# Kernel tuning notes

Measured on AMD Instinct MI355X. Metric: run time of the kernel, lower is better.

## Reference

```python
import math
import jax, jax.numpy as jnp
import numpy as np

E = 1024
H = 16
HD = E // H
MLP = 4 * E
EPS = 1e-6


def setup_inputs() -> dict:
    key = jax.random.key(0)
    ks = jax.random.split(key, 12)
    s = lambda fan_in: 1.0 / math.sqrt(fan_in)
    return {
        "x": jax.random.normal(ks[0], (8, 1024, E), dtype=jnp.float32),
        "ln1_g": jnp.ones((E,), jnp.float32),
        "ln1_b": jnp.zeros((E,), jnp.float32),
        "w_qkv": jax.random.normal(ks[1], (E, 3 * E), jnp.float32) * s(E),
        "b_qkv": jnp.zeros((3 * E,), jnp.float32),
        "w_o": jax.random.normal(ks[2], (E, E), jnp.float32) * s(E),
        "b_o": jnp.zeros((E,), jnp.float32),
        "ln2_g": jnp.ones((E,), jnp.float32),
        "ln2_b": jnp.zeros((E,), jnp.float32),
        "w_fc1": jax.random.normal(ks[3], (E, MLP), jnp.float32) * s(E),
        "b_fc1": jnp.zeros((MLP,), jnp.float32),
        "w_fc2": jax.random.normal(ks[4], (MLP, E), jnp.float32) * s(MLP),
        "b_fc2": jnp.zeros((E,), jnp.float32),
    }


def _layernorm(x, g, b):
    mu = jnp.mean(x, axis=-1, keepdims=True)
    var = jnp.mean(jnp.square(x - mu), axis=-1, keepdims=True)
    return (x - mu) * jax.lax.rsqrt(var + EPS) * g + b


def _attn(x, w_qkv, b_qkv, w_o, b_o):
    B, N, _ = x.shape
    qkv = (x @ w_qkv + b_qkv).reshape(B, N, 3, H, HD)
    q, k, v = qkv[:, :, 0], qkv[:, :, 1], qkv[:, :, 2]  # [B,N,H,HD]
    scores = jnp.einsum("bnhd,bmhd->bhnm", q, k) / math.sqrt(HD)
    probs = jax.nn.softmax(scores, axis=-1)
    out = jnp.einsum("bhnm,bmhd->bnhd", probs, v).reshape(B, N, H * HD)
    return out @ w_o + b_o


def reference(x, ln1_g, ln1_b, w_qkv, b_qkv, w_o, b_o, ln2_g, ln2_b,
              w_fc1, b_fc1, w_fc2, b_fc2):
    # pre-LN attention block with residual
    x = x + _attn(_layernorm(x, ln1_g, ln1_b), w_qkv, b_qkv, w_o, b_o)
    # pre-LN MLP block with residual (exact GELU, matching torch nn.GELU)
    h = _layernorm(x, ln2_g, ln2_b) @ w_fc1 + b_fc1
    h = jax.nn.gelu(h, approximate=False)
    x = x + (h @ w_fc2 + b_fc2)
    return x
```

## Files before the change

kernel.cpp:

```cpp
#include <hip/hip_runtime.h>
#include <stdint.h>

typedef unsigned short u16;
typedef __bf16 bf16x8 __attribute__((ext_vector_type(8)));
typedef float f32x4 __attribute__((ext_vector_type(4)));

#define GLD16(gp, lp) __builtin_amdgcn_global_load_lds( \
    (__attribute__((address_space(1))) void*)(uintptr_t)(gp), \
    (__attribute__((address_space(3))) void*)(uintptr_t)(lp), 16, 0, 0)

#define MM(a, b, c) __builtin_amdgcn_mfma_f32_16x16x32_bf16(a, b, c, 0, 0, 0)

__device__ __forceinline__ u16 f2bf(float f) {
  uint32_t u = __builtin_bit_cast(uint32_t, f);
  u += 0x7FFFu + ((u >> 16) & 1u);
  return (u16)(u >> 16);
}

__global__ __launch_bounds__(256) void wtrans(const float* __restrict__ w,
                                              u16* __restrict__ wt, int K, int Nn) {
  __shared__ float tile[64][68];
  const int c0 = blockIdx.x << 6, r0 = blockIdx.y << 6;
  const int t = threadIdx.x, tr = t >> 2, tc = t & 3;
#pragma unroll
  for (int p = 0; p < 4; ++p) {
    float4 v = *(const float4*)&w[(size_t)(r0 + tr) * Nn + c0 + tc * 4 + p * 16];
    tile[tr][tc * 4 + p * 16 + 0] = v.x;
    tile[tr][tc * 4 + p * 16 + 1] = v.y;
    tile[tr][tc * 4 + p * 16 + 2] = v.z;
    tile[tr][tc * 4 + p * 16 + 3] = v.w;
  }
  __syncthreads();
#pragma unroll
  for (int p = 0; p < 4; ++p) {
    u16 e0 = f2bf(tile[tc * 4 + p * 16 + 0][tr]);
    u16 e1 = f2bf(tile[tc * 4 + p * 16 + 1][tr]);
    u16 e2 = f2bf(tile[tc * 4 + p * 16 + 2][tr]);
    u16 e3 = f2bf(tile[tc * 4 + p * 16 + 3][tr]);
    uint2 o;
    o.x = (uint32_t)e0 | ((uint32_t)e1 << 16);
    o.y = (uint32_t)e2 | ((uint32_t)e3 << 16);
    *(uint2*)&wt[(size_t)(c0 + tr) * K + r0 + tc * 4 + p * 16] = o;
  }
}

__global__ __launch_bounds__(256) void lnorm(const float* x, const float* __restrict__ g,
                                             const float* __restrict__ bta,
                                             u16* __restrict__ out) {
  const int lane = threadIdx.x & 63, wid = threadIdx.x >> 6;
  const size_t token = (size_t)blockIdx.x * 4 + wid;
  const float* row = x + token * 1024;
  float v[16];
#pragma unroll
  for (int i = 0; i < 4; ++i) {
    float4 f = *(const float4*)&row[(lane + i * 64) * 4];
    v[i * 4 + 0] = f.x; v[i * 4 + 1] = f.y; v[i * 4 + 2] = f.z; v[i * 4 + 3] = f.w;
  }
  float s = 0.f, s2 = 0.f;
#pragma unroll
  for (int i = 0; i < 16; ++i) { s += v[i]; s2 += v[i] * v[i]; }
  for (int off = 1; off < 64; off <<= 1) {
    s += __shfl_xor(s, off);
    s2 += __shfl_xor(s2, off);
  }
  const float mu = s * (1.0f / 1024.0f);
  const float var = s2 * (1.0f / 1024.0f) - mu * mu;
  const float rstd = rsqrtf(var + 1e-6f);
  u16* orow = out + token * 1024;
#pragma unroll
  for (int i = 0; i < 4; ++i) {
    const int c = (lane + i * 64) * 4;
    float4 gv = *(const float4*)&g[c];
    float4 bv = *(const float4*)&bta[c];
    u16 e0 = f2bf((v[i * 4 + 0] - mu) * rstd * gv.x + bv.x);
    u16 e1 = f2bf((v[i * 4 + 1] - mu) * rstd * gv.y + bv.y);
    u16 e2 = f2bf((v[i * 4 + 2] - mu) * rstd * gv.z + bv.z);
    u16 e3 = f2bf((v[i * 4 + 3] - mu) * rstd * gv.w + bv.w);
    uint2 o;
    o.x = (uint32_t)e0 | ((uint32_t)e1 << 16);
    o.y = (uint32_t)e2 | ((uint32_t)e3 << 16);
    *(uint2*)&orow[c] = o;
  }
}

template <int EPI>
__global__ __launch_bounds__(256, 2) void g97(const u16* __restrict__ A,
                                              const u16* __restrict__ Bt,
                                              const float* __restrict__ bias,
                                              const float* res, void* Cout,
                                              int Ndim, int K, float qscale,
                                              int qlimit, int gn) {
  __shared__ __align__(16) u16 lds[2][16384];
  const int tid = threadIdx.x, lane = tid & 63, wid = tid >> 6;
  const int wm = wid & 1, wn = wid >> 1;

  const int wg = blockIdx.x;
  const int swz = (wg & 7) * ((int)gridDim.x >> 3) + (wg >> 3);
  const int mblk = swz / gn, nb = swz - mblk * gn;
  const int m0 = mblk << 7, n0 = nb << 7;

  const int srow = tid >> 3;
  const int schunk = (tid & 7) ^ (srow & 7);
  const u16* Ag = A + (size_t)(m0 + srow) * K + schunk * 8;
  const u16* Bg = Bt + (size_t)(n0 + srow) * K + schunk * 8;
  const size_t rstep = (size_t)32 * K;
  char* lb = (char*)&lds[0][0];

  const int rrow = lane & 15, g = lane >> 4;
  const int ph0 = (g ^ (rrow & 7)) * 16;
  const int aoff0 = (wm * 64 + rrow) * 128 + ph0;
  const int aoff1 = (wm * 64 + rrow) * 128 + (ph0 ^ 64);
  const int boff0 = 16384 + (wn * 64 + rrow) * 128 + ph0;
  const int boff1 = 16384 + (wn * 64 + rrow) * 128 + (ph0 ^ 64);

  const f32x4 fzero = {0.f, 0.f, 0.f, 0.f};
  f32x4 acc[4][4];
#pragma unroll
  for (int i = 0; i < 4; ++i)
#pragma unroll
    for (int j = 0; j < 4; ++j) acc[i][j] = fzero;

#define STG(kt, s) do { \
    char* d_ = lb + (s) * 32768; \
    const u16* a_ = Ag + (size_t)(kt) * 64; \
    const u16* b_ = Bg + (size_t)(kt) * 64; \
    GLD16(a_,             d_ + tid * 16); \
    GLD16(a_ + rstep,     d_ + 4096 + tid * 16); \
    GLD16(a_ + 2 * rstep, d_ + 8192 + tid * 16); \
    GLD16(a_ + 3 * rstep, d_ + 12288 + tid * 16); \
    GLD16(b_,             d_ + 16384 + tid * 16); \
    GLD16(b_ + rstep,     d_ + 20480 + tid * 16); \
    GLD16(b_ + 2 * rstep, d_ + 24576 + tid * 16); \
    GLD16(b_ + 3 * rstep, d_ + 28672 + tid * 16); \
  } while (0)

  const int nk = K >> 6;
  STG(0, 0);
  __syncthreads();
  for (int kt = 0; kt < nk; ++kt) {
    if (kt + 1 < nk) STG(kt + 1, (kt + 1) & 1);
    const char* sb = lb + (kt & 1) * 32768;
    bf16x8 af[4], bfr[4];
#pragma unroll
    for (int mf = 0; mf < 4; ++mf)
      af[mf] = *(const bf16x8*)(sb + aoff0 + mf * 2048);
#pragma unroll
    for (int nf = 0; nf < 4; ++nf)
      bfr[nf] = *(const bf16x8*)(sb + boff0 + nf * 2048);
#pragma unroll
    for (int mf = 0; mf < 4; ++mf)
#pragma unroll
      for (int nf = 0; nf < 4; ++nf)
        acc[mf][nf] = MM(af[mf], bfr[nf], acc[mf][nf]);
#pragma unroll
    for (int mf = 0; mf < 4; ++mf)
      af[mf] = *(const bf16x8*)(sb + aoff1 + mf * 2048);
#pragma unroll
    for (int nf = 0; nf < 4; ++nf)
      bfr[nf] = *(const bf16x8*)(sb + boff1 + nf * 2048);
#pragma unroll
    for (int mf = 0; mf < 4; ++mf)
#pragma unroll
      for (int nf = 0; nf < 4; ++nf)
        acc[mf][nf] = MM(af[mf], bfr[nf], acc[mf][nf]);
    __syncthreads();
  }
#undef STG

  const int g4 = (lane >> 4) << 2;
#pragma unroll
  for (int nf = 0; nf < 4; ++nf) {
    const int col = n0 + wn * 64 + nf * 16 + rrow;
    const float bvb = bias[col];
    const float csf = (EPI == 0 && col < qlimit) ? qscale : 1.0f;
#pragma unroll
    for (int mf = 0; mf < 4; ++mf) {
#pragma unroll
      for (int r = 0; r < 4; ++r) {
        const int row = m0 + wm * 64 + mf * 16 + g4 + r;
        float v = acc[mf][nf][r] + bvb;
        if (EPI == 0) v *= csf;
        if (EPI == 1) v = 0.5f * v * (1.0f + erff(v * 0.70710678118654752f));
        if (EPI == 2) {
          v += res[(size_t)row * Ndim + col];
          ((float*)Cout)[(size_t)row * Ndim + col] = v;
        } else {
          ((u16*)Cout)[(size_t)row * Ndim + col] = f2bf(v);
        }
      }
    }
  }
}

__global__ __launch_bounds__(256) void vtrans(const u16* __restrict__ qkv,
                                              u16* __restrict__ vt) {
  const int bh = blockIdx.y, b = bh >> 4, h = bh & 15;
  const int n0 = blockIdx.x << 6;
  __shared__ __align__(16) u16 tile[64][72];
  const int t = threadIdx.x, r = t >> 2, c = t & 3;
  const u16* src = qkv + (size_t)((b << 10) + n0 + r) * 3072 + 2048 + (h << 6);
#pragma unroll
  for (int p = 0; p < 2; ++p)
    *(uint4*)&tile[r][(c * 2 + p) * 8] = *(const uint4*)(src + (c * 2 + p) * 8);
  __syncthreads();
  u16* dst = vt + (size_t)((bh << 6) + r) * 1024 + n0;
#pragma unroll
  for (int p = 0; p < 2; ++p) {
    u16 o[8];
#pragma unroll
    for (int j = 0; j < 8; ++j) o[j] = tile[(c * 2 + p) * 8 + j][r];
    uint4 w;
    w.x = (uint32_t)o[0] | ((uint32_t)o[1] << 16);
    w.y = (uint32_t)o[2] | ((uint32_t)o[3] << 16);
    w.z = (uint32_t)o[4] | ((uint32_t)o[5] << 16);
    w.w = (uint32_t)o[6] | ((uint32_t)o[7] << 16);
    *(uint4*)&dst[(c * 2 + p) * 8] = w;
  }
}

__global__ __launch_bounds__(256) void attn64(const u16* __restrict__ qkv,
                                              const u16* __restrict__ vt,
                                              u16* __restrict__ aout) {
  const int bh = blockIdx.y, b = bh >> 4, h = bh & 15;
  const int q0 = blockIdx.x << 6;
  const int tid = threadIdx.x, lane = tid & 63, wid = tid >> 6;
  __shared__ __align__(16) u16 kl[4096];
  __shared__ __align__(16) u16 vl[4096];
  __shared__ __align__(16) u16 pl[4][1152];

  const int rrow = lane & 15;
  const int g = lane >> 4;
  const u16* qrow = qkv + (size_t)((b << 10) + q0 + (wid << 4) + rrow) * 3072 + (h << 6);
  bf16x8 qf0 = *(const bf16x8*)(qrow + (g << 3));
  bf16x8 qf1 = *(const bf16x8*)(qrow + 32 + (g << 3));

  const int sr = lane >> 3;
  const int lc = (lane & 7) ^ sr;
  const u16* kbase = qkv + (size_t)(b << 10) * 3072 + 1024 + (h << 6) +
                     (size_t)(16 * wid + sr) * 3072 + lc * 8;
  const u16* vbase = vt + (size_t)(bh << 6) * 1024 + (size_t)(16 * wid + sr) * 1024 + lc * 8;

  const f32x4 fzero = {0.f, 0.f, 0.f, 0.f};
  f32x4 oacc[4];
#pragma unroll
  for (int i = 0; i < 4; ++i) oacc[i] = fzero;
  f32x4 lacc = fzero;
  const int rcb = lane & 7;
  u16* plw = &pl[wid][0];

  for (int t = 0; t < 16; ++t) {
    const int kt0 = t << 6;
    GLD16(kbase + (size_t)kt0 * 3072, &kl[(2 * wid + 0) * 512]);
    GLD16(kbase + (size_t)kt0 * 3072 + 8 * 3072, &kl[(2 * wid + 1) * 512]);
    GLD16(vbase + kt0, &vl[(2 * wid + 0) * 512]);
    GLD16(vbase + kt0 + 8 * 1024, &vl[(2 * wid + 1) * 512]);
    __syncthreads();

    f32x4 s4[4];
#pragma unroll
    for (int i = 0; i < 4; ++i) s4[i] = fzero;
#pragma unroll
    for (int nf = 0; nf < 4; ++nf) {
      bf16x8 k0 = *(const bf16x8*)((const char*)kl + (nf * 16 + rrow) * 128 +
                                   ((g + 0) ^ rcb) * 16);
      bf16x8 k1 = *(const bf16x8*)((const char*)kl + (nf * 16 + rrow) * 128 +
                                   ((g + 4) ^ rcb) * 16);
      s4[nf] = __builtin_amdgcn_mfma_f32_16x16x32_bf16(k0, qf0, s4[nf], 0, 0, 0);
      s4[nf] = __builtin_amdgcn_mfma_f32_16x16x32_bf16(k1, qf1, s4[nf], 0, 0, 0);
    }

#pragma unroll
    for (int nf = 0; nf < 4; ++nf) {
      float p0 = exp2f(s4[nf][0]);
      float p1 = exp2f(s4[nf][1]);
      float p2 = exp2f(s4[nf][2]);
      float p3 = exp2f(s4[nf][3]);
      f32x4 pv = {p0, p1, p2, p3};
      lacc += pv;
      uint32_t a0 = __builtin_bit_cast(uint32_t, p0) + 0x8000u;
      uint32_t a1 = __builtin_bit_cast(uint32_t, p1) + 0x8000u;
      uint32_t a2 = __builtin_bit_cast(uint32_t, p2) + 0x8000u;
      uint32_t a3 = __builtin_bit_cast(uint32_t, p3) + 0x8000u;
      uint2 w;
      w.x = __builtin_amdgcn_perm(a1, a0, 0x07060302);
      w.y = __builtin_amdgcn_perm(a3, a2, 0x07060302);
      *(uint2*)(plw + rrow * 72 + nf * 16 + (g << 2)) = w;
    }

    bf16x8 pf0 = *(const bf16x8*)((const char*)plw + rrow * 144 + (g << 4));
    bf16x8 pf1 = *(const bf16x8*)((const char*)plw + rrow * 144 + (g << 4) + 64);
#pragma unroll
    for (int nf = 0; nf < 4; ++nf) {
      bf16x8 v0 = *(const bf16x8*)((const char*)vl + (nf * 16 + rrow) * 128 +
                                   ((g + 0) ^ rcb) * 16);
      bf16x8 v1 = *(const bf16x8*)((const char*)vl + (nf * 16 + rrow) * 128 +
                                   ((g + 4) ^ rcb) * 16);
      oacc[nf] = __builtin_amdgcn_mfma_f32_16x16x32_bf16(pf0, v0, oacc[nf], 0, 0, 0);
      oacc[nf] = __builtin_amdgcn_mfma_f32_16x16x32_bf16(pf1, v1, oacc[nf], 0, 0, 0);
    }
    __syncthreads();
  }

  float lsum = lacc[0] + lacc[1] + lacc[2] + lacc[3];
  lsum += __shfl_xor(lsum, 16);
  lsum += __shfl_xor(lsum, 32);
  const float inv = 1.0f / lsum;
  float invq[4];
#pragma unroll
  for (int r = 0; r < 4; ++r) {
    int bi = __builtin_amdgcn_ds_bpermute(((g << 2) + r) << 2,
                                          __builtin_bit_cast(int, inv));
    invq[r] = __builtin_bit_cast(float, bi);
  }
  u16* ob = aout + (size_t)((b << 10) + q0 + (wid << 4)) * 1024 + (h << 6);
#pragma unroll
  for (int nf = 0; nf < 4; ++nf)
#pragma unroll
    for (int r = 0; r < 4; ++r)
      ob[(size_t)(g * 4 + r) * 1024 + nf * 16 + rrow] = f2bf(oacc[nf][r] * invq[r]);
}

extern "C" void kernel_launch(void* const* d_in, const int* in_sizes, int n_in,
                              void* d_out, int out_size, void* d_ws, size_t ws_size,
                              hipStream_t stream) {
  const float* x = (const float*)d_in[0];
  const float* ln1_g = (const float*)d_in[1];
  const float* ln1_b = (const float*)d_in[2];
  const float* w_qkv = (const float*)d_in[3];
  const float* b_qkv = (const float*)d_in[4];
  const float* w_o = (const float*)d_in[5];
  const float* b_o = (const float*)d_in[6];
  const float* ln2_g = (const float*)d_in[7];
  const float* ln2_b = (const float*)d_in[8];
  const float* w_fc1 = (const float*)d_in[9];
  const float* b_fc1 = (const float*)d_in[10];
  const float* w_fc2 = (const float*)d_in[11];
  const float* b_fc2 = (const float*)d_in[12];
  float* out = (float*)d_out;

  char* w = (char*)d_ws;
  u16* wqkvT = (u16*)w; w += (size_t)3072 * 1024 * 2;
  u16* woT   = (u16*)w; w += (size_t)1024 * 1024 * 2;
  u16* wfc1T = (u16*)w; w += (size_t)4096 * 1024 * 2;
  u16* wfc2T = (u16*)w; w += (size_t)1024 * 4096 * 2;
  u16* xn    = (u16*)w; w += (size_t)8192 * 1024 * 2;
  u16* qkvb  = (u16*)w; w += (size_t)8192 * 3072 * 2;
  u16* vtb   = (u16*)w; w += (size_t)128 * 64 * 1024 * 2;
  u16* attnb = (u16*)w; w += (size_t)8192 * 1024 * 2;
  u16* hbuf  = qkvb;

  const float QS = 0.18033688011112042f;

  wtrans<<<dim3(48, 16), 256, 0, stream>>>(w_qkv, wqkvT, 1024, 3072);
  wtrans<<<dim3(16, 16), 256, 0, stream>>>(w_o, woT, 1024, 1024);
  wtrans<<<dim3(64, 16), 256, 0, stream>>>(w_fc1, wfc1T, 1024, 4096);
  wtrans<<<dim3(16, 64), 256, 0, stream>>>(w_fc2, wfc2T, 4096, 1024);

  lnorm<<<2048, 256, 0, stream>>>(x, ln1_g, ln1_b, xn);
  g97<0><<<1536, 256, 0, stream>>>(xn, wqkvT, b_qkv, nullptr, qkvb, 3072, 1024, QS, 1024, 24);
  vtrans<<<dim3(16, 128), 256, 0, stream>>>(qkvb, vtb);
  attn64<<<dim3(16, 128), 256, 0, stream>>>(qkvb, vtb, attnb);
  g97<2><<<512, 256, 0, stream>>>(attnb, woT, b_o, x, out, 1024, 1024, 1.f, 0, 8);
  lnorm<<<2048, 256, 0, stream>>>(out, ln2_g, ln2_b, xn);
  g97<1><<<2048, 256, 0, stream>>>(xn, wfc1T, b_fc1, nullptr, hbuf, 4096, 1024, 1.f, 0, 32);
  g97<2><<<512, 256, 0, stream>>>(hbuf, wfc2T, b_fc2, out, out, 1024, 4096, 1.f, 0, 8);
}
```

Baseline: 408.6 us.

## Add 256x256 eight-wave pipelined GEMM for QKV/FC1 and double-buffer attention K/V

Adds a new 512-thread GEMM kernel with 256x256 tiles, double-buffered LDS, and interleaved quarter-stage prefetch using explicit vmcnt waits, barriers and setprio. It replaces the 128x128 kernel for the QKV and FC1 projections. The goal is more data reuse per tile and better overlap of global loads with MFMA work. The attention kernel now double-buffers K/V tiles so the next tile loads while the current one is computed. The old GEMM is kept only for the residual-add epilogues. The trade-off is one block per CU, higher LDS and register use, and fewer blocks in the grid.

```diff
diff --git a/kernel.cpp b/kernel.cpp
--- a/kernel.cpp
+++ b/kernel.cpp
@@ -9,6 +9,8 @@
     (__attribute__((address_space(1))) void*)(uintptr_t)(gp), \
     (__attribute__((address_space(3))) void*)(uintptr_t)(lp), 16, 0, 0)
 
+#define WAITVM(N) asm volatile("s_waitcnt vmcnt(" #N ")" ::: "memory")
+#define BAR() __builtin_amdgcn_s_barrier()
 #define MM(a, b, c) __builtin_amdgcn_mfma_f32_16x16x32_bf16(a, b, c, 0, 0, 0)
 
 __device__ __forceinline__ u16 f2bf(float f) {
@@ -84,12 +86,172 @@
 }
 
 template <int EPI>
+__global__ __launch_bounds__(512, 1) void g8p(const u16* __restrict__ A,
+                                              const u16* __restrict__ Bt,
+                                              const float* __restrict__ bias,
+                                              u16* __restrict__ Cout,
+                                              int Ndim, int K, float qscale,
+                                              int qlimit, int gn) {
+  __shared__ __align__(16) u16 lds[2][32768];
+  const int tid = threadIdx.x, lane = tid & 63, wid = tid >> 6;
+  const int wm = wid >> 2, wn = wid & 3;
+
+  const int wg = blockIdx.x;
+  const int swz = (wg & 7) * ((int)gridDim.x >> 3) + (wg >> 3);
+  const int mblk = swz / gn, nb = swz - mblk * gn;
+  const int m0 = mblk << 8, n0 = nb << 8;
+
+  const int srow = tid >> 3;
+  const int sch = (tid & 7) ^ (srow & 7);
+  const u16* Ag = A + (size_t)(m0 + srow) * K + sch * 8;
+  const u16* Bg = Bt + (size_t)(n0 + srow) * K + sch * 8;
+  const size_t r64 = (size_t)64 * K;
+  char* lb = (char*)&lds[0][0];
+
+  const int rrow = lane & 15, g = lane >> 4;
+  const int xk0 = (g ^ (rrow & 7)) << 4;
+  const int xk1 = ((4 | g) ^ (rrow & 7)) << 4;
+  const char* pAs[2];
+  const char* pBs[2];
+#pragma unroll
+  for (int s = 0; s < 2; ++s) {
+    pAs[s] = lb + s * 65536 + wm * 16384 + rrow * 128;
+    pBs[s] = lb + s * 65536 + 32768 + (wn >> 1) * 16384 + ((wn & 1) * 64 + rrow) * 128;
+  }
+
+  const f32x4 fz = {0.f, 0.f, 0.f, 0.f};
+  f32x4 acc[8][4];
+#pragma unroll
+  for (int i = 0; i < 8; ++i)
+#pragma unroll
+    for (int j = 0; j < 4; ++j) acc[i][j] = fz;
+
+#define STG_H(kt, ss, half, base) do { \
+    const u16* p_ = (base) + (size_t)(kt) * 64; \
+    char* d_ = lb + (ss) * 65536 + (half) * 16384 + tid * 16; \
+    GLD16(p_, d_); \
+    GLD16(p_ + r64, d_ + 8192); \
+  } while (0)
+
+  const int nT = K >> 6;
+  STG_H(0, 0, 0, Ag);
+  STG_H(0, 0, 1, Ag + 2 * r64);
+  STG_H(0, 0, 2, Bg);
+  STG_H(0, 0, 3, Bg + 2 * r64);
+  WAITVM(0);
+  BAR();
+
+  for (int t = 0; t < nT; ++t) {
+    const int s = t & 1, ss = s ^ 1;
+    const char* pa = pAs[s];
+    const char* pb = pBs[s];
+    const bool st = (t + 1 < nT);
+    bf16x8 a[4][2], b[2][2];
+#pragma unroll
+    for (int i = 0; i < 4; ++i) {
+      a[i][0] = *(const bf16x8*)(pa + i * 2048 + xk0);
+      a[i][1] = *(const bf16x8*)(pa + i * 2048 + xk1);
+    }
+#pragma unroll
+    for (int j = 0; j < 2; ++j) {
+      b[j][0] = *(const bf16x8*)(pb + j * 2048 + xk0);
+      b[j][1] = *(const bf16x8*)(pb + j * 2048 + xk1);
+    }
+    if (st) STG_H(t + 1, ss, 0, Ag);
+    WAITVM(4);
+    BAR();
+    __builtin_amdgcn_s_setprio(1);
+#pragma unroll
+    for (int i = 0; i < 4; ++i)
+#pragma unroll
+      for (int j = 0; j < 2; ++j) {
+        acc[i][j] = MM(a[i][0], b[j][0], acc[i][j]);
+        acc[i][j] = MM(a[i][1], b[j][1], acc[i][j]);
+      }
+    __builtin_amdgcn_s_setprio(0);
+    BAR();
+#pragma unroll
+    for (int i = 0; i < 4; ++i) {
+      a[i][0] = *(const bf16x8*)(pa + (4 + i) * 2048 + xk0);
+      a[i][1] = *(const bf16x8*)(pa + (4 + i) * 2048 + xk1);
+    }
+    if (st) STG_H(t + 1, ss, 2, Bg);
+    WAITVM(4);
+    BAR();
+    __builtin_amdgcn_s_setprio(1);
+#pragma unroll
+    for (int i = 0; i < 4; ++i)
+#pragma unroll
+      for (int j = 0; j < 2; ++j) {
+        acc[4 + i][j] = MM(a[i][0], b[j][0], acc[4 + i][j]);
+        acc[4 + i][j] = MM(a[i][1], b[j][1], acc[4 + i][j]);
+      }
+    __builtin_amdgcn_s_setprio(0);
+    BAR();
+#pragma unroll
+    for (int j = 0; j < 2; ++j) {
+      b[j][0] = *(const bf16x8*)(pb + (2 + j) * 2048 + xk0);
+      b[j][1] = *(const bf16x8*)(pb + (2 + j) * 2048 + xk1);
+    }
+    if (st) STG_H(t + 1, ss, 1, Ag + 2 * r64);
+    WAITVM(4);
+    BAR();
+    __builtin_amdgcn_s_setprio(1);
+#pragma unroll
+    for (int i = 0; i < 4; ++i)
+#pragma unroll
+      for (int j = 0; j < 2; ++j) {
+        acc[4 + i][2 + j] = MM(a[i][0], b[j][0], acc[4 + i][2 + j]);
+        acc[4 + i][2 + j] = MM(a[i][1], b[j][1], acc[4 + i][2 + j]);
+      }
+    __builtin_amdgcn_s_setprio(0);
+    BAR();
+#pragma unroll
+    for (int i = 0; i < 4; ++i) {
+      a[i][0] = *(const bf16x8*)(pa + i * 2048 + xk0);
+      a[i][1] = *(const bf16x8*)(pa + i * 2048 + xk1);
+    }
+    if (st) STG_H(t + 1, ss, 3, Bg + 2 * r64);
+    WAITVM(4);
+    BAR();
+    __builtin_amdgcn_s_setprio(1);
+#pragma unroll
+    for (int i = 0; i < 4; ++i)
+#pragma unroll
+      for (int j = 0; j < 2; ++j) {
+        acc[i][2 + j] = MM(a[i][0], b[j][0], acc[i][2 + j]);
+        acc[i][2 + j] = MM(a[i][1], b[j][1], acc[i][2 + j]);
+      }
+    __builtin_amdgcn_s_setprio(0);
+    BAR();
+  }
+#undef STG_H
+
+  const int g4 = g << 2;
+#pragma unroll
+  for (int nf = 0; nf < 4; ++nf) {
+    const int col = n0 + wn * 64 + nf * 16 + rrow;
+    const float bvb = bias[col];
+    const float csf = (EPI == 0 && col < qlimit) ? qscale : 1.0f;
+#pragma unroll
+    for (int mf = 0; mf < 8; ++mf) {
+#pragma unroll
+      for (int r = 0; r < 4; ++r) {
+        const int row = m0 + wm * 128 + mf * 16 + g4 + r;
+        float v = acc[mf][nf][r] + bvb;
+        if (EPI == 0) v *= csf;
+        if (EPI == 1) v = 0.5f * v * (1.0f + erff(v * 0.70710678118654752f));
+        Cout[(size_t)row * Ndim + col] = f2bf(v);
+      }
+    }
+  }
+}
+
 __global__ __launch_bounds__(256, 2) void g97(const u16* __restrict__ A,
                                               const u16* __restrict__ Bt,
                                               const float* __restrict__ bias,
-                                              const float* res, void* Cout,
-                                              int Ndim, int K, float qscale,
-                                              int qlimit, int gn) {
+                                              const float* res, float* Cout,
+                                              int Ndim, int K, int gn) {
   __shared__ __align__(16) u16 lds[2][16384];
   const int tid = threadIdx.x, lane = tid & 63, wid = tid >> 6;
   const int wm = wid & 1, wn = wid >> 1;
@@ -172,21 +334,13 @@
   for (int nf = 0; nf < 4; ++nf) {
     const int col = n0 + wn * 64 + nf * 16 + rrow;
     const float bvb = bias[col];
-    const float csf = (EPI == 0 && col < qlimit) ? qscale : 1.0f;
 #pragma unroll
     for (int mf = 0; mf < 4; ++mf) {
 #pragma unroll
       for (int r = 0; r < 4; ++r) {
         const int row = m0 + wm * 64 + mf * 16 + g4 + r;
-        float v = acc[mf][nf][r] + bvb;
-        if (EPI == 0) v *= csf;
-        if (EPI == 1) v = 0.5f * v * (1.0f + erff(v * 0.70710678118654752f));
-        if (EPI == 2) {
-          v += res[(size_t)row * Ndim + col];
-          ((float*)Cout)[(size_t)row * Ndim + col] = v;
-        } else {
-          ((u16*)Cout)[(size_t)row * Ndim + col] = f2bf(v);
-        }
+        float v = acc[mf][nf][r] + bvb + res[(size_t)row * Ndim + col];
+        Cout[(size_t)row * Ndim + col] = v;
       }
     }
   }
@@ -224,8 +378,8 @@
   const int bh = blockIdx.y, b = bh >> 4, h = bh & 15;
   const int q0 = blockIdx.x << 6;
   const int tid = threadIdx.x, lane = tid & 63, wid = tid >> 6;
-  __shared__ __align__(16) u16 kl[4096];
-  __shared__ __align__(16) u16 vl[4096];
+  __shared__ __align__(16) u16 kl[2][4096];
+  __shared__ __align__(16) u16 vl[2][4096];
   __shared__ __align__(16) u16 pl[4][1152];
 
   const int rrow = lane & 15;
@@ -248,23 +402,28 @@
   const int rcb = lane & 7;
   u16* plw = &pl[wid][0];
 
+#define ASTAGE(t, s) do { \
+    const int kt0_ = (t) << 6; \
+    GLD16(kbase + (size_t)kt0_ * 3072, &kl[s][(2 * wid + 0) * 512]); \
+    GLD16(kbase + (size_t)kt0_ * 3072 + 8 * 3072, &kl[s][(2 * wid + 1) * 512]); \
+    GLD16(vbase + kt0_, &vl[s][(2 * wid + 0) * 512]); \
+    GLD16(vbase + kt0_ + 8 * 1024, &vl[s][(2 * wid + 1) * 512]); \
+  } while (0)
+
+  ASTAGE(0, 0);
+  __syncthreads();
   for (int t = 0; t < 16; ++t) {
-    const int kt0 = t << 6;
-    GLD16(kbase + (size_t)kt0 * 3072, &kl[(2 * wid + 0) * 512]);
-    GLD16(kbase + (size_t)kt0 * 3072 + 8 * 3072, &kl[(2 * wid + 1) * 512]);
-    GLD16(vbase + kt0, &vl[(2 * wid + 0) * 512]);
-    GLD16(vbase + kt0 + 8 * 1024, &vl[(2 * wid + 1) * 512]);
-    __syncthreads();
+    if (t + 1 < 16) ASTAGE(t + 1, (t + 1) & 1);
+    const char* klp = (const char*)&kl[t & 1][0];
+    const char* vlp = (const char*)&vl[t & 1][0];
 
     f32x4 s4[4];
 #pragma unroll
     for (int i = 0; i < 4; ++i) s4[i] = fzero;
 #pragma unroll
     for (int nf = 0; nf < 4; ++nf) {
-      bf16x8 k0 = *(const bf16x8*)((const char*)kl + (nf * 16 + rrow) * 128 +
-                                   ((g + 0) ^ rcb) * 16);
-      bf16x8 k1 = *(const bf16x8*)((const char*)kl + (nf * 16 + rrow) * 128 +
-                                   ((g + 4) ^ rcb) * 16);
+      bf16x8 k0 = *(const bf16x8*)(klp + (nf * 16 + rrow) * 128 + ((g + 0) ^ rcb) * 16);
+      bf16x8 k1 = *(const bf16x8*)(klp + (nf * 16 + rrow) * 128 + ((g + 4) ^ rcb) * 16);
       s4[nf] = __builtin_amdgcn_mfma_f32_16x16x32_bf16(k0, qf0, s4[nf], 0, 0, 0);
       s4[nf] = __builtin_amdgcn_mfma_f32_16x16x32_bf16(k1, qf1, s4[nf], 0, 0, 0);
     }
@@ -291,15 +450,14 @@
     bf16x8 pf1 = *(const bf16x8*)((const char*)plw + rrow * 144 + (g << 4) + 64);
 #pragma unroll
     for (int nf = 0; nf < 4; ++nf) {
-      bf16x8 v0 = *(const bf16x8*)((const char*)vl + (nf * 16 + rrow) * 128 +
-                                   ((g + 0) ^ rcb) * 16);
-      bf16x8 v1 = *(const bf16x8*)((const char*)vl + (nf * 16 + rrow) * 128 +
-                                   ((g + 4) ^ rcb) * 16);
+      bf16x8 v0 = *(const bf16x8*)(vlp + (nf * 16 + rrow) * 128 + ((g + 0) ^ rcb) * 16);
+      bf16x8 v1 = *(const bf16x8*)(vlp + (nf * 16 + rrow) * 128 + ((g + 4) ^ rcb) * 16);
       oacc[nf] = __builtin_amdgcn_mfma_f32_16x16x32_bf16(pf0, v0, oacc[nf], 0, 0, 0);
       oacc[nf] = __builtin_amdgcn_mfma_f32_16x16x32_bf16(pf1, v1, oacc[nf], 0, 0, 0);
     }
     __syncthreads();
   }
+#undef ASTAGE
 
   float lsum = lacc[0] + lacc[1] + lacc[2] + lacc[3];
   lsum += __shfl_xor(lsum, 16);
@@ -357,11 +515,11 @@
   wtrans<<<dim3(16, 64), 256, 0, stream>>>(w_fc2, wfc2T, 4096, 1024);
 
   lnorm<<<2048, 256, 0, stream>>>(x, ln1_g, ln1_b, xn);
-  g97<0><<<1536, 256, 0, stream>>>(xn, wqkvT, b_qkv, nullptr, qkvb, 3072, 1024, QS, 1024, 24);
+  g8p<0><<<384, 512, 0, stream>>>(xn, wqkvT, b_qkv, qkvb, 3072, 1024, QS, 1024, 12);
   vtrans<<<dim3(16, 128), 256, 0, stream>>>(qkvb, vtb);
   attn64<<<dim3(16, 128), 256, 0, stream>>>(qkvb, vtb, attnb);
-  g97<2><<<512, 256, 0, stream>>>(attnb, woT, b_o, x, out, 1024, 1024, 1.f, 0, 8);
+  g97<<<512, 256, 0, stream>>>(attnb, woT, b_o, x, out, 1024, 1024, 8);
   lnorm<<<2048, 256, 0, stream>>>(out, ln2_g, ln2_b, xn);
-  g97<1><<<2048, 256, 0, stream>>>(xn, wfc1T, b_fc1, nullptr, hbuf, 4096, 1024, 1.f, 0, 32);
-  g97<2><<<512, 256, 0, stream>>>(hbuf, wfc2T, b_fc2, out, out, 1024, 4096, 1.f, 0, 8);
-}
+  g8p<1><<<512, 512, 0, stream>>>(xn, wfc1T, b_fc1, hbuf, 4096, 1024, 1.f, 0, 16);
+  g97<<<512, 256, 0, stream>>>(hbuf, wfc2T, b_fc2, out, out, 1024, 4096, 8);
+}
```

Result: slower. 561.3 us (+37.4%).

## Double-buffer K/V tiles in attention and raise wave priority around MFMAs

Applied to the files above, without the earlier changes.

The attention kernel now keeps two LDS buffers for K and V. While the MFMAs for tile t run on one buffer, the global-to-LDS loads for tile t+1 go into the other, so one barrier per iteration is removed from the critical path and load latency overlaps with compute. It also wraps the MFMA loops in s_setprio so waves doing matrix math are scheduled ahead of others. The cost is twice the K/V LDS footprint, which may lower occupancy, and correctness relies on the end-of-loop barrier waiting for the outstanding async loads.

```diff
diff --git a/kernel.cpp b/kernel.cpp
--- a/kernel.cpp
+++ b/kernel.cpp
@@ -224,8 +224,8 @@
   const int bh = blockIdx.y, b = bh >> 4, h = bh & 15;
   const int q0 = blockIdx.x << 6;
   const int tid = threadIdx.x, lane = tid & 63, wid = tid >> 6;
-  __shared__ __align__(16) u16 kl[4096];
-  __shared__ __align__(16) u16 vl[4096];
+  __shared__ __align__(16) u16 kl[2][4096];
+  __shared__ __align__(16) u16 vl[2][4096];
   __shared__ __align__(16) u16 pl[4][1152];
 
   const int rrow = lane & 15;
@@ -248,26 +248,33 @@
   const int rcb = lane & 7;
   u16* plw = &pl[wid][0];
 
+#define ASTAGE(t, s) do { \
+    const int kt0_ = (t) << 6; \
+    GLD16(kbase + (size_t)kt0_ * 3072, &kl[s][(2 * wid + 0) * 512]); \
+    GLD16(kbase + (size_t)kt0_ * 3072 + 8 * 3072, &kl[s][(2 * wid + 1) * 512]); \
+    GLD16(vbase + kt0_, &vl[s][(2 * wid + 0) * 512]); \
+    GLD16(vbase + kt0_ + 8 * 1024, &vl[s][(2 * wid + 1) * 512]); \
+  } while (0)
+
+  ASTAGE(0, 0);
+  __syncthreads();
   for (int t = 0; t < 16; ++t) {
-    const int kt0 = t << 6;
-    GLD16(kbase + (size_t)kt0 * 3072, &kl[(2 * wid + 0) * 512]);
-    GLD16(kbase + (size_t)kt0 * 3072 + 8 * 3072, &kl[(2 * wid + 1) * 512]);
-    GLD16(vbase + kt0, &vl[(2 * wid + 0) * 512]);
-    GLD16(vbase + kt0 + 8 * 1024, &vl[(2 * wid + 1) * 512]);
-    __syncthreads();
+    if (t + 1 < 16) ASTAGE(t + 1, (t + 1) & 1);
+    const char* klp = (const char*)&kl[t & 1][0];
+    const char* vlp = (const char*)&vl[t & 1][0];
 
     f32x4 s4[4];
 #pragma unroll
     for (int i = 0; i < 4; ++i) s4[i] = fzero;
+    __builtin_amdgcn_s_setprio(1);
 #pragma unroll
     for (int nf = 0; nf < 4; ++nf) {
-      bf16x8 k0 = *(const bf16x8*)((const char*)kl + (nf * 16 + rrow) * 128 +
-                                   ((g + 0) ^ rcb) * 16);
-      bf16x8 k1 = *(const bf16x8*)((const char*)kl + (nf * 16 + rrow) * 128 +
-                                   ((g + 4) ^ rcb) * 16);
+      bf16x8 k0 = *(const bf16x8*)(klp + (nf * 16 + rrow) * 128 + ((g + 0) ^ rcb) * 16);
+      bf16x8 k1 = *(const bf16x8*)(klp + (nf * 16 + rrow) * 128 + ((g + 4) ^ rcb) * 16);
       s4[nf] = __builtin_amdgcn_mfma_f32_16x16x32_bf16(k0, qf0, s4[nf], 0, 0, 0);
       s4[nf] = __builtin_amdgcn_mfma_f32_16x16x32_bf16(k1, qf1, s4[nf], 0, 0, 0);
     }
+    __builtin_amdgcn_s_setprio(0);
 
 #pragma unroll
     for (int nf = 0; nf < 4; ++nf) {
@@ -289,17 +296,18 @@
 
     bf16x8 pf0 = *(const bf16x8*)((const char*)plw + rrow * 144 + (g << 4));
     bf16x8 pf1 = *(const bf16x8*)((const char*)plw + rrow * 144 + (g << 4) + 64);
+    __builtin_amdgcn_s_setprio(1);
 #pragma unroll
     for (int nf = 0; nf < 4; ++nf) {
-      bf16x8 v0 = *(const bf16x8*)((const char*)vl + (nf * 16 + rrow) * 128 +
-                                   ((g + 0) ^ rcb) * 16);
-      bf16x8 v1 = *(const bf16x8*)((const char*)vl + (nf * 16 + rrow) * 128 +
-                                   ((g + 4) ^ rcb) * 16);
+      bf16x8 v0 = *(const bf16x8*)(vlp + (nf * 16 + rrow) * 128 + ((g + 0) ^ rcb) * 16);
+      bf16x8 v1 = *(const bf16x8*)(vlp + (nf * 16 + rrow) * 128 + ((g + 4) ^ rcb) * 16);
       oacc[nf] = __builtin_amdgcn_mfma_f32_16x16x32_bf16(pf0, v0, oacc[nf], 0, 0, 0);
       oacc[nf] = __builtin_amdgcn_mfma_f32_16x16x32_bf16(pf1, v1, oacc[nf], 0, 0, 0);
     }
+    __builtin_amdgcn_s_setprio(0);
     __syncthreads();
   }
+#undef ASTAGE
 
   float lsum = lacc[0] + lacc[1] + lacc[2] + lacc[3];
   lsum += __shfl_xor(lsum, 16);
```

Measured after the change: 409.4 us. Within noise of the previous version (+0.2%).
